# Performance work log

Measured on AMD Instinct MI355X. Metric: run time of the kernel, lower is better.

Reference implementation:

```python
import jax, jax.numpy as jnp
import numpy as np
from jax.ops import segment_sum, segment_max

N, E = 50000, 500000
F_IN, H, D1, D2, EDIM, HID = 388, 8, 64, 128, 16, 32


def gatv2(x, edge_index, edge_attr, Wl, Wr, We, att, bias, concat):
    # PyG GATv2Conv with edge_dim, add_self_loops=True, fill_value='mean', eval mode (no dropout)
    n = x.shape[0]
    h, d = att.shape
    src, dst = edge_index[0], edge_index[1]
    deg = segment_sum(jnp.ones(src.shape, x.dtype), dst, num_segments=n)
    loop_attr = segment_sum(edge_attr, dst, num_segments=n) / jnp.maximum(deg, 1.0)[:, None]
    loops = jnp.arange(n)
    src = jnp.concatenate([src, loops])
    dst = jnp.concatenate([dst, loops])
    ea = jnp.concatenate([edge_attr, loop_attr], axis=0)
    xl = (x @ Wl).reshape(n, h, d)   # source transform (lin_l)
    xr = (x @ Wr).reshape(n, h, d)   # target transform (lin_r)
    ee = (ea @ We).reshape(-1, h, d)
    m = jax.nn.leaky_relu(xl[src] + xr[dst] + ee, 0.2)   # [E+N, h, d]
    score = jnp.einsum('ehd,hd->eh', m, att)              # [E+N, h]
    smax = segment_max(score, dst, num_segments=n)        # every node has a self-loop
    alpha = jnp.exp(score - smax[dst])
    denom = segment_sum(alpha, dst, num_segments=n)
    alpha = alpha / denom[dst]
    out = segment_sum(alpha[:, :, None] * xl[src], dst, num_segments=n)  # [n, h, d]
    out = out.reshape(n, h * d) if concat else out.mean(axis=1)
    return out + bias


def setup_inputs():
    key = jax.random.key(0)
    ks = jax.random.split(key, 24)
    p = lambda k, shape: (jax.random.normal(k, shape, jnp.float32) * 0.05)
    return {
        'x': jax.random.normal(ks[0], (N, F_IN), jnp.float32),
        'edge_index': jax.random.randint(ks[1], (2, E), 0, N),
        'edge_attr': jax.random.normal(ks[2], (E, EDIM), jnp.float32),
        'Wl1': p(ks[3], (F_IN, H * D1)), 'Wr1': p(ks[4], (F_IN, H * D1)),
        'We1': p(ks[5], (EDIM, H * D1)), 'att1': p(ks[6], (H, D1)), 'b1': p(ks[7], (H * D1,)),
        'Wl2': p(ks[8], (H * D1, H * D2)), 'Wr2': p(ks[9], (H * D1, H * D2)),
        'We2': p(ks[10], (EDIM, H * D2)), 'att2': p(ks[11], (H, D2)), 'b2': p(ks[12], (D2,)),
        'W_ih': p(ks[13], (4 * HID, D2)), 'W_hh': p(ks[14], (4 * HID, HID)),
        'b_ih': p(ks[15], (4 * HID,)), 'b_hh': p(ks[16], (4 * HID,)),
        'fcW': p(ks[17], (1, HID)), 'fcb': p(ks[18], (1,)),
    }


def reference(x, edge_index, edge_attr, Wl1, Wr1, We1, att1, b1,
              Wl2, Wr2, We2, att2, b2, W_ih, W_hh, b_ih, b_hh, fcW, fcb):
    h = jnp.tanh(gatv2(x, edge_index, edge_attr, Wl1, Wr1, We1, att1, b1, True))
    h = jnp.tanh(gatv2(h, edge_index, edge_attr, Wl2, Wr2, We2, att2, b2, False))
    # single-step LSTM, h0=c0=0; W_hh @ h0 == 0 but biases remain
    gates = h @ W_ih.T + b_ih + b_hh                      # [N, 4*HID]
    i, f, g, o = jnp.split(gates, 4, axis=1)
    c = jax.nn.sigmoid(i) * jnp.tanh(g)
    hidden = jax.nn.sigmoid(o) * jnp.tanh(c)              # [N, HID]
    return hidden @ fcW.T + fcb                           # [N, 1]
```

## Files before the change

### kernel.cpp

```cpp
#include <hip/hip_runtime.h>

#define N_NODES 50000
#define N_EDGES 500000
#define F_INDIM 388
#define H_HEADS 8
#define DD1 64
#define DD2 128
#define EDIM 16
#define HIDN 32

#define M_PAD 50048
#define K1_PAD 416

typedef unsigned short u16;
typedef unsigned int u32;
typedef __attribute__((ext_vector_type(8))) short bf16x8;
typedef __attribute__((ext_vector_type(4))) float f32x4;

static __device__ __forceinline__ float bfu2f(u32 lo16) {
  union { u32 u; float f; } c;
  c.u = lo16 << 16;
  return c.f;
}
static __device__ __forceinline__ u16 f2bf(float f) {
  union { float f; u32 u; } c;
  c.f = f;
  u32 u = c.u + 0x7fffu + ((c.u >> 16) & 1u);
  return (u16)(u >> 16);
}

static __device__ __forceinline__ float waveSum(float v) {
#pragma unroll
  for (int off = 32; off > 0; off >>= 1) v += __shfl_xor(v, off, 64);
  return v;
}
static __device__ __forceinline__ void waveSum4(float& a, float& b, float& c, float& d) {
#pragma unroll
  for (int off = 32; off > 0; off >>= 1) {
    a += __shfl_xor(a, off, 64);
    b += __shfl_xor(b, off, 64);
    c += __shfl_xor(c, off, 64);
    d += __shfl_xor(d, off, 64);
  }
}

static __device__ __forceinline__ void gl_lds16(const void* g, void* l) {
  __builtin_amdgcn_global_load_lds((const __attribute__((address_space(1))) u32*)g,
                                   (__attribute__((address_space(3))) u32*)l, 16, 0, 0);
}

__global__ void k_zero(float* __restrict__ out, int n) {
  int i = blockIdx.x * blockDim.x + threadIdx.x;
  if (i < n) out[i] = 0.f;
}

__global__ void k_hist(const int* __restrict__ dst, int* __restrict__ deg) {
  int e = blockIdx.x * blockDim.x + threadIdx.x;
  if (e < N_EDGES) atomicAdd(&deg[dst[e]], 1);
}

__global__ __launch_bounds__(1024) void k_scan(const int* __restrict__ deg,
                                               int* __restrict__ row_start) {
  __shared__ int wsum[16];
  __shared__ int carry_s;
  int tid = threadIdx.x;
  int lane = tid & 63, wv = tid >> 6;
  if (tid == 0) carry_s = 0;
  __syncthreads();
  for (int base = 0; base < N_NODES; base += 1024) {
    int i = base + tid;
    int v = (i < N_NODES) ? deg[i] : 0;
    int inc = v;
#pragma unroll
    for (int off = 1; off < 64; off <<= 1) {
      int t = __shfl_up(inc, off, 64);
      if (lane >= off) inc += t;
    }
    if (lane == 63) wsum[wv] = inc;
    __syncthreads();
    if (wv == 0 && lane < 16) {
      int s = wsum[lane];
#pragma unroll
      for (int off = 1; off < 16; off <<= 1) {
        int t = __shfl_up(s, off, 64);
        if (lane >= off) s += t;
      }
      wsum[lane] = s;
    }
    __syncthreads();
    int add = (wv > 0) ? wsum[wv - 1] : 0;
    int ex = carry_s + add + inc - v;
    if (i < N_NODES) row_start[i] = ex;
    __syncthreads();
    if (tid == 0) carry_s += wsum[15];
    __syncthreads();
  }
  if (threadIdx.x == 0) row_start[N_NODES] = carry_s;
}

__global__ void k_scatter(const int* __restrict__ dst, const int* __restrict__ src,
                          const int* __restrict__ row_start, int* __restrict__ cursor,
                          int* __restrict__ eid, int* __restrict__ srcp) {
  int e = blockIdx.x * blockDim.x + threadIdx.x;
  if (e < N_EDGES) {
    int d = dst[e];
    int pos = row_start[d] + atomicAdd(&cursor[d], 1);
    eid[pos] = e;
    srcp[pos] = src[e];
  }
}

__global__ void k_cvt_x(const float* __restrict__ x, u16* __restrict__ xb) {
  long t = (long)blockIdx.x * 256 + threadIdx.x;
  if (t >= (long)M_PAD * K1_PAD) return;
  int row = (int)(t / K1_PAD);
  int col = (int)(t % K1_PAD);
  float v = (row < N_NODES && col < F_INDIM) ? x[(size_t)row * F_INDIM + col] : 0.f;
  xb[t] = f2bf(v);
}

__global__ void k_cvt_wT(const float* __restrict__ W, u16* __restrict__ WT, int K, int N, int Kp) {
  int t = blockIdx.x * 256 + threadIdx.x;
  if (t >= N * Kp) return;
  int n = t / Kp, k = t % Kp;
  WT[t] = f2bf(k < K ? W[(size_t)k * N + n] : 0.f);
}

__global__ void k_cvt(const float* __restrict__ W, u16* __restrict__ O, int n) {
  int t = blockIdx.x * 256 + threadIdx.x;
  if (t < n) O[t] = f2bf(W[t]);
}

template <bool CF32>
__global__ __launch_bounds__(256) void gemm_mfma(const u16* __restrict__ A,
                                                 const u16* __restrict__ BT,
                                                 void* __restrict__ Cv, int M, int Nd, int K,
                                                 int lda, int ldb) {
  __shared__ u16 As[128 * 32];
  __shared__ u16 Bs[128 * 32];
  int tid = threadIdx.x;
  int lane = tid & 63;
  int wv = tid >> 6;
  int m_base = blockIdx.y * 128;
  int n_base = blockIdx.x * 128;
  int wrow = (wv >> 1) * 64;
  int wcol = (wv & 1) * 64;
  f32x4 acc[4][4];
#pragma unroll
  for (int i = 0; i < 4; ++i)
#pragma unroll
    for (int j = 0; j < 4; ++j)
#pragma unroll
      for (int r = 0; r < 4; ++r) acc[i][j][r] = 0.f;

  for (int k0 = 0; k0 < K; k0 += 32) {
    __syncthreads();
#pragma unroll
    for (int it = 0; it < 2; ++it) {
      int t = it * 256 + tid;
      int row = t >> 2;
      int kc = (t & 3) * 8;
      gl_lds16(A + (size_t)(m_base + row) * lda + k0 + kc, As + (size_t)(it * 256 + wv * 64) * 8);
      gl_lds16(BT + (size_t)(n_base + row) * ldb + k0 + kc, Bs + (size_t)(it * 256 + wv * 64) * 8);
    }
    __syncthreads();
    bf16x8 af[4], bfr[4];
#pragma unroll
    for (int i = 0; i < 4; ++i) {
      int r = wrow + i * 16 + (lane & 15);
      af[i] = *(const bf16x8*)(As + r * 32 + (lane >> 4) * 8);
    }
#pragma unroll
    for (int j = 0; j < 4; ++j) {
      int r = wcol + j * 16 + (lane & 15);
      bfr[j] = *(const bf16x8*)(Bs + r * 32 + (lane >> 4) * 8);
    }
#pragma unroll
    for (int i = 0; i < 4; ++i)
#pragma unroll
      for (int j = 0; j < 4; ++j)
        acc[i][j] = __builtin_amdgcn_mfma_f32_16x16x32_bf16(af[i], bfr[j], acc[i][j], 0, 0, 0);
  }
#pragma unroll
  for (int i = 0; i < 4; ++i) {
    int grow_base = m_base + wrow + i * 16 + (lane >> 4) * 4;
#pragma unroll
    for (int j = 0; j < 4; ++j) {
      int gcol = n_base + wcol + j * 16 + (lane & 15);
#pragma unroll
      for (int r = 0; r < 4; ++r) {
        int grow = grow_base + r;
        if (grow < M) {
          float v = acc[i][j][r];
          if (CF32)
            ((float*)Cv)[(size_t)grow * Nd + gcol] = v;
          else
            ((u16*)Cv)[(size_t)grow * Nd + gcol] = f2bf(v);
        }
      }
    }
  }
}

__global__ __launch_bounds__(512) void k_gat1(
    const u16* __restrict__ xl, const u16* __restrict__ xr, const float* __restrict__ ea,
    const float* __restrict__ We, const float* __restrict__ att, const float* __restrict__ bias,
    const int* __restrict__ srcp, const int* __restrict__ eid, const int* __restrict__ row_start,
    u16* __restrict__ out) {
  const int NC = H_HEADS * DD1;
  int n = blockIdx.x;
  int tid = threadIdx.x;
  int lane = tid & 63;
  int h = tid >> 6;
  __shared__ float laP[512];
  __shared__ float la[EDIM];
  int r0 = row_start[n], r1 = row_start[n + 1];
  int deg = r1 - r0;

  {
    int k = tid & 15, i0 = tid >> 4;
    float s = 0.f;
    for (int i = i0; i < deg; i += 32) s += ea[(size_t)eid[r0 + i] * EDIM + k];
    laP[tid] = s;
  }

  int col = h * DD1 + lane;
  float Wc[EDIM];
#pragma unroll
  for (int k = 0; k < EDIM; ++k) Wc[k] = We[k * NC + col];
  float attd = att[col];
  float xrd = bfu2f(xr[(size_t)n * NC + col]);
  float xlself = bfu2f(xl[(size_t)n * NC + col]);

  auto escore = [&](int e, float xv) -> float {
    const float4* ea4 = (const float4*)(ea + (size_t)e * EDIM);
    float4 v0 = ea4[0], v1 = ea4[1], v2 = ea4[2], v3 = ea4[3];
    float eacc = v0.x * Wc[0];
    eacc = fmaf(v0.y, Wc[1], eacc);
    eacc = fmaf(v0.z, Wc[2], eacc);
    eacc = fmaf(v0.w, Wc[3], eacc);
    eacc = fmaf(v1.x, Wc[4], eacc);
    eacc = fmaf(v1.y, Wc[5], eacc);
    eacc = fmaf(v1.z, Wc[6], eacc);
    eacc = fmaf(v1.w, Wc[7], eacc);
    eacc = fmaf(v2.x, Wc[8], eacc);
    eacc = fmaf(v2.y, Wc[9], eacc);
    eacc = fmaf(v2.z, Wc[10], eacc);
    eacc = fmaf(v2.w, Wc[11], eacc);
    eacc = fmaf(v3.x, Wc[12], eacc);
    eacc = fmaf(v3.y, Wc[13], eacc);
    eacc = fmaf(v3.z, Wc[14], eacc);
    eacc = fmaf(v3.w, Wc[15], eacc);
    float zz = xv + xrd + eacc;
    float mm = zz > 0.f ? zz : 0.2f * zz;
    return mm * attd;
  };

  float acc = 0.f, denom = 0.f;
  int i = r0;
  for (; i + 4 <= r1; i += 4) {
    int e0 = eid[i], e1 = eid[i + 1], e2 = eid[i + 2], e3 = eid[i + 3];
    int s0 = srcp[i], s1 = srcp[i + 1], s2 = srcp[i + 2], s3 = srcp[i + 3];
    float x0 = bfu2f(xl[(size_t)s0 * NC + col]);
    float x1 = bfu2f(xl[(size_t)s1 * NC + col]);
    float x2 = bfu2f(xl[(size_t)s2 * NC + col]);
    float x3 = bfu2f(xl[(size_t)s3 * NC + col]);
    float p0 = escore(e0, x0);
    float p1 = escore(e1, x1);
    float p2 = escore(e2, x2);
    float p3 = escore(e3, x3);
    waveSum4(p0, p1, p2, p3);
    float w0 = __expf(p0), w1 = __expf(p1), w2 = __expf(p2), w3 = __expf(p3);
    acc = fmaf(w0, x0, acc);
    acc = fmaf(w1, x1, acc);
    acc = fmaf(w2, x2, acc);
    acc = fmaf(w3, x3, acc);
    denom += (w0 + w1) + (w2 + w3);
  }
  for (; i < r1; ++i) {
    int e = eid[i];
    int s = srcp[i];
    float xv = bfu2f(xl[(size_t)s * NC + col]);
    float p = waveSum(escore(e, xv));
    float ww = __expf(p);
    acc = fmaf(ww, xv, acc);
    denom += ww;
  }

  __syncthreads();
  if (tid < EDIM) {
    float s = 0.f;
#pragma unroll
    for (int g = 0; g < 32; ++g) s += laP[g * 16 + tid];
    la[tid] = s / (float)max(deg, 1);
  }
  __syncthreads();
  float ee = 0.f;
#pragma unroll
  for (int k = 0; k < EDIM; ++k) ee = fmaf(la[k], Wc[k], ee);
  float z = xlself + xrd + ee;
  float m = z > 0.f ? z : 0.2f * z;
  float sc = waveSum(m * attd);
  float w = __expf(sc);
  acc = fmaf(w, xlself, acc);
  denom += w;

  out[(size_t)n * NC + col] = f2bf(tanhf(acc / denom + bias[col]));
}

__global__ __launch_bounds__(512) void k_gat2(
    const u16* __restrict__ xl, const u16* __restrict__ xr, const float* __restrict__ ea,
    const float* __restrict__ We, const float* __restrict__ att, const float* __restrict__ bias,
    const int* __restrict__ srcp, const int* __restrict__ eid, const int* __restrict__ row_start,
    u16* __restrict__ out) {
  const int NC = H_HEADS * DD2;
  int n = blockIdx.x;
  int tid = threadIdx.x;
  int lane = tid & 63;
  int h = tid >> 6;
  __shared__ float laP[512];
  __shared__ float la[EDIM];
  __shared__ float hsum[H_HEADS][DD2];
  int r0 = row_start[n], r1 = row_start[n + 1];
  int deg = r1 - r0;

  {
    int k = tid & 15, i0 = tid >> 4;
    float s = 0.f;
    for (int i = i0; i < deg; i += 32) s += ea[(size_t)eid[r0 + i] * EDIM + k];
    laP[tid] = s;
  }

  int col = h * DD2 + lane * 2;
  float Wcx[EDIM], Wcy[EDIM];
#pragma unroll
  for (int k = 0; k < EDIM; ++k) {
    float2 t = *(const float2*)(We + k * NC + col);
    Wcx[k] = t.x;
    Wcy[k] = t.y;
  }
  float2 attd = *(const float2*)(att + col);
  u32 xru = *(const u32*)(xr + (size_t)n * NC + col);
  u32 xlu = *(const u32*)(xl + (size_t)n * NC + col);
  float xrdx = bfu2f(xru & 0xffff), xrdy = bfu2f(xru >> 16);
  float xlsx = bfu2f(xlu & 0xffff), xlsy = bfu2f(xlu >> 16);

  auto escore2 = [&](int e, float xvx, float xvy) -> float {
    const float4* ea4 = (const float4*)(ea + (size_t)e * EDIM);
    float4 v0 = ea4[0], v1 = ea4[1], v2 = ea4[2], v3 = ea4[3];
    float ex = v0.x * Wcx[0], ey = v0.x * Wcy[0];
    ex = fmaf(v0.y, Wcx[1], ex); ey = fmaf(v0.y, Wcy[1], ey);
    ex = fmaf(v0.z, Wcx[2], ex); ey = fmaf(v0.z, Wcy[2], ey);
    ex = fmaf(v0.w, Wcx[3], ex); ey = fmaf(v0.w, Wcy[3], ey);
    ex = fmaf(v1.x, Wcx[4], ex); ey = fmaf(v1.x, Wcy[4], ey);
    ex = fmaf(v1.y, Wcx[5], ex); ey = fmaf(v1.y, Wcy[5], ey);
    ex = fmaf(v1.z, Wcx[6], ex); ey = fmaf(v1.z, Wcy[6], ey);
    ex = fmaf(v1.w, Wcx[7], ex); ey = fmaf(v1.w, Wcy[7], ey);
    ex = fmaf(v2.x, Wcx[8], ex); ey = fmaf(v2.x, Wcy[8], ey);
    ex = fmaf(v2.y, Wcx[9], ex); ey = fmaf(v2.y, Wcy[9], ey);
    ex = fmaf(v2.z, Wcx[10], ex); ey = fmaf(v2.z, Wcy[10], ey);
    ex = fmaf(v2.w, Wcx[11], ex); ey = fmaf(v2.w, Wcy[11], ey);
    ex = fmaf(v3.x, Wcx[12], ex); ey = fmaf(v3.x, Wcy[12], ey);
    ex = fmaf(v3.y, Wcx[13], ex); ey = fmaf(v3.y, Wcy[13], ey);
    ex = fmaf(v3.z, Wcx[14], ex); ey = fmaf(v3.z, Wcy[14], ey);
    ex = fmaf(v3.w, Wcx[15], ex); ey = fmaf(v3.w, Wcy[15], ey);
    float zx = xvx + xrdx + ex, zy = xvy + xrdy + ey;
    float mx = zx > 0.f ? zx : 0.2f * zx, my = zy > 0.f ? zy : 0.2f * zy;
    return mx * attd.x + my * attd.y;
  };

  float accx = 0.f, accy = 0.f, denom = 0.f;
  int i = r0;
  for (; i + 4 <= r1; i += 4) {
    int e0 = eid[i], e1 = eid[i + 1], e2 = eid[i + 2], e3 = eid[i + 3];
    int s0 = srcp[i], s1 = srcp[i + 1], s2 = srcp[i + 2], s3 = srcp[i + 3];
    u32 u0 = *(const u32*)(xl + (size_t)s0 * NC + col);
    u32 u1 = *(const u32*)(xl + (size_t)s1 * NC + col);
    u32 u2 = *(const u32*)(xl + (size_t)s2 * NC + col);
    u32 u3 = *(const u32*)(xl + (size_t)s3 * NC + col);
    float x0x = bfu2f(u0 & 0xffff), x0y = bfu2f(u0 >> 16);
    float x1x = bfu2f(u1 & 0xffff), x1y = bfu2f(u1 >> 16);
    float x2x = bfu2f(u2 & 0xffff), x2y = bfu2f(u2 >> 16);
    float x3x = bfu2f(u3 & 0xffff), x3y = bfu2f(u3 >> 16);
    float p0 = escore2(e0, x0x, x0y);
    float p1 = escore2(e1, x1x, x1y);
    float p2 = escore2(e2, x2x, x2y);
    float p3 = escore2(e3, x3x, x3y);
    waveSum4(p0, p1, p2, p3);
    float w0 = __expf(p0), w1 = __expf(p1), w2 = __expf(p2), w3 = __expf(p3);
    accx = fmaf(w0, x0x, accx); accy = fmaf(w0, x0y, accy);
    accx = fmaf(w1, x1x, accx); accy = fmaf(w1, x1y, accy);
    accx = fmaf(w2, x2x, accx); accy = fmaf(w2, x2y, accy);
    accx = fmaf(w3, x3x, accx); accy = fmaf(w3, x3y, accy);
    denom += (w0 + w1) + (w2 + w3);
  }
  for (; i < r1; ++i) {
    int e = eid[i];
    int s = srcp[i];
    u32 u0 = *(const u32*)(xl + (size_t)s * NC + col);
    float xvx = bfu2f(u0 & 0xffff), xvy = bfu2f(u0 >> 16);
    float p = waveSum(escore2(e, xvx, xvy));
    float ww = __expf(p);
    accx = fmaf(ww, xvx, accx);
    accy = fmaf(ww, xvy, accy);
    denom += ww;
  }

  __syncthreads();
  if (tid < EDIM) {
    float s = 0.f;
#pragma unroll
    for (int g = 0; g < 32; ++g) s += laP[g * 16 + tid];
    la[tid] = s / (float)max(deg, 1);
  }
  __syncthreads();
  float eex = 0.f, eey = 0.f;
#pragma unroll
  for (int k = 0; k < EDIM; ++k) {
    eex = fmaf(la[k], Wcx[k], eex);
    eey = fmaf(la[k], Wcy[k], eey);
  }
  float zx = xlsx + xrdx + eex, zy = xlsy + xrdy + eey;
  float mx = zx > 0.f ? zx : 0.2f * zx, my = zy > 0.f ? zy : 0.2f * zy;
  float sc = waveSum(mx * attd.x + my * attd.y);
  float w = __expf(sc);
  accx = fmaf(w, xlsx, accx);
  accy = fmaf(w, xlsy, accy);
  denom += w;

  float inv = 1.f / denom;
  hsum[h][lane * 2] = accx * inv;
  hsum[h][lane * 2 + 1] = accy * inv;
  __syncthreads();
  if (tid < DD2) {
    float s = 0.f;
#pragma unroll
    for (int hh = 0; hh < H_HEADS; ++hh) s += hsum[hh][tid];
    out[(size_t)n * DD2 + tid] = f2bf(tanhf(s * 0.125f + bias[tid]));
  }
}

__global__ __launch_bounds__(128) void k_lstm(const float* __restrict__ gates,
                                              const float* __restrict__ b_ih,
                                              const float* __restrict__ b_hh,
                                              const float* __restrict__ fcW,
                                              const float* __restrict__ fcb,
                                              float* __restrict__ out) {
  int n = blockIdx.x;
  int j = threadIdx.x;
  __shared__ float gs[128];
  gs[j] = gates[(size_t)n * 128 + j] + b_ih[j] + b_hh[j];
  __syncthreads();
  if (j < 32) {
    float iv = gs[j], gv = gs[64 + j], ov = gs[96 + j];
    float c = (1.f / (1.f + __expf(-iv))) * tanhf(gv);
    float hd = (1.f / (1.f + __expf(-ov))) * tanhf(c);
    float p = hd * fcW[j];
#pragma unroll
    for (int off = 16; off > 0; off >>= 1) p += __shfl_down(p, off, 32);
    if (j == 0) out[n] = p + fcb[0];
  }
}

extern "C" void kernel_launch(void* const* d_in, const int* in_sizes, int n_in, void* d_out,
                              int out_size, void* d_ws, size_t ws_size, hipStream_t stream) {
  const float* x = (const float*)d_in[0];
  const int* ei = (const int*)d_in[1];
  const float* ea = (const float*)d_in[2];
  const float* Wl1 = (const float*)d_in[3];
  const float* Wr1 = (const float*)d_in[4];
  const float* We1 = (const float*)d_in[5];
  const float* att1 = (const float*)d_in[6];
  const float* b1 = (const float*)d_in[7];
  const float* Wl2 = (const float*)d_in[8];
  const float* Wr2 = (const float*)d_in[9];
  const float* We2 = (const float*)d_in[10];
  const float* att2 = (const float*)d_in[11];
  const float* b2 = (const float*)d_in[12];
  const float* W_ih = (const float*)d_in[13];
  const float* b_ih = (const float*)d_in[15];
  const float* b_hh = (const float*)d_in[16];
  const float* fcW = (const float*)d_in[17];
  const float* fcb = (const float*)d_in[18];
  float* out = (float*)d_out;
  const int* srcA = ei;
  const int* dstA = ei + N_EDGES;

  char* ws = (char*)d_ws;
  const size_t SZ_XL1 = (size_t)N_NODES * 512 * 2;
  const size_t SZ_P0 = (size_t)N_NODES * 1024 * 2;
  const size_t SZ_P1 = SZ_P0;
  const size_t SZ_H1 = (size_t)M_PAD * 512 * 2;
  const size_t SZ_H2 = (size_t)M_PAD * 128 * 2;
  size_t P0 = 0;
  size_t P1 = P0 + SZ_P0;
  size_t P2 = P1 + SZ_P1;
  size_t P3 = P2 + SZ_H1;
  size_t off = P3;
  auto take = [&](size_t bytes) -> char* {
    off = (off + 255) & ~(size_t)255;
    char* p = ws + off;
    off += bytes;
    return p;
  };
  u16* W1lT = (u16*)take((size_t)512 * K1_PAD * 2);
  u16* W1rT = (u16*)take((size_t)512 * K1_PAD * 2);
  u16* W2lT = (u16*)take((size_t)1024 * 512 * 2);
  u16* W2rT = (u16*)take((size_t)1024 * 512 * 2);
  u16* WihB = (u16*)take((size_t)128 * 128 * 2);
  int* deg = (int*)take((size_t)N_NODES * 4);
  int* cursor = (int*)take((size_t)N_NODES * 4);
  int* row_start = (int*)take((size_t)(N_NODES + 1) * 4);
  int* eid = (int*)take((size_t)N_EDGES * 4);
  int* srcp = (int*)take((size_t)N_EDGES * 4);

  if (off > ws_size) {
    k_zero<<<(out_size + 255) / 256, 256, 0, stream>>>(out, out_size);
    return;
  }

  u16* xl1 = (u16*)(ws + P0);
  u16* xr1 = (u16*)(ws + P0 + SZ_XL1);
  u16* xl2 = (u16*)(ws + P0);
  u16* xbf = (u16*)(ws + P1);
  u16* xr2 = (u16*)(ws + P1);
  u16* h1 = (u16*)(ws + P2);
  u16* h2 = (u16*)(ws + P2);
  float* gates = (float*)(ws + P2 + SZ_H2);

  hipMemsetAsync(deg, 0, (size_t)N_NODES * 4, stream);
  hipMemsetAsync(cursor, 0, (size_t)N_NODES * 4, stream);
  k_hist<<<(N_EDGES + 255) / 256, 256, 0, stream>>>(dstA, deg);
  k_scan<<<1, 1024, 0, stream>>>(deg, row_start);
  k_scatter<<<(N_EDGES + 255) / 256, 256, 0, stream>>>(dstA, srcA, row_start, cursor, eid, srcp);

  {
    long tot = (long)M_PAD * K1_PAD;
    k_cvt_x<<<(unsigned)((tot + 255) / 256), 256, 0, stream>>>(x, xbf);
    k_cvt_wT<<<(512 * K1_PAD + 255) / 256, 256, 0, stream>>>(Wl1, W1lT, F_INDIM, 512, K1_PAD);
    k_cvt_wT<<<(512 * K1_PAD + 255) / 256, 256, 0, stream>>>(Wr1, W1rT, F_INDIM, 512, K1_PAD);
    k_cvt_wT<<<(1024 * 512 + 255) / 256, 256, 0, stream>>>(Wl2, W2lT, 512, 1024, 512);
    k_cvt_wT<<<(1024 * 512 + 255) / 256, 256, 0, stream>>>(Wr2, W2rT, 512, 1024, 512);
    k_cvt<<<(128 * 128 + 255) / 256, 256, 0, stream>>>(W_ih, WihB, 128 * 128);
  }

  const int MB = M_PAD / 128;
  {
    dim3 g(512 / 128, MB);
    gemm_mfma<false><<<g, 256, 0, stream>>>(xbf, W1lT, xl1, N_NODES, 512, K1_PAD, K1_PAD, K1_PAD);
    gemm_mfma<false><<<g, 256, 0, stream>>>(xbf, W1rT, xr1, N_NODES, 512, K1_PAD, K1_PAD, K1_PAD);
  }
  k_gat1<<<N_NODES, 512, 0, stream>>>(xl1, xr1, ea, We1, att1, b1, srcp, eid, row_start, h1);

  {
    dim3 g(1024 / 128, MB);
    gemm_mfma<false><<<g, 256, 0, stream>>>(h1, W2lT, xl2, N_NODES, 1024, 512, 512, 512);
    gemm_mfma<false><<<g, 256, 0, stream>>>(h1, W2rT, xr2, N_NODES, 1024, 512, 512, 512);
  }
  k_gat2<<<N_NODES, 512, 0, stream>>>(xl2, xr2, ea, We2, att2, b2, srcp, eid, row_start, h2);

  {
    dim3 g(1, MB);
    gemm_mfma<true><<<g, 256, 0, stream>>>(h2, WihB, gates, N_NODES, 128, 128, 128, 128);
  }
  k_lstm<<<N_NODES, 128, 0, stream>>>(gates, b_ih, b_hh, fcW, fcb, out);
}
```

Baseline: 1.576 ms.

## Fuse lin_l/lin_r GEMMs, precompute self-loop edge means, prefetch neighbor gathers

The separate left and right projection GEMMs are merged into one GEMM over concatenated weights, writing an interleaved xl|xr buffer. The per-node mean of edge attributes for self-loops is computed once in a new kernel and shared by both GAT layers, which removes the per-block reduction and its two barriers. The GAT edge loops now use scalar (readfirstlane) edge indices, software-prefetch the next four neighbor rows, and express leaky_relu as 0.6*z+0.4*|z|. The cost is extra register pressure and a wider row stride in the gathered feature buffer.

```diff
diff --git a/kernel.cpp b/kernel.cpp
--- a/kernel.cpp
+++ b/kernel.cpp
@@ -108,6 +108,19 @@
     eid[pos] = e;
     srcp[pos] = src[e];
   }
+}
+
+__global__ __launch_bounds__(256) void k_la(const float* __restrict__ ea,
+                                            const int* __restrict__ eid,
+                                            const int* __restrict__ row_start,
+                                            float* __restrict__ la) {
+  int node = blockIdx.x * 16 + (threadIdx.x >> 4);
+  int k = threadIdx.x & 15;
+  if (node >= N_NODES) return;
+  int r0 = row_start[node], r1 = row_start[node + 1];
+  float s = 0.f;
+  for (int i = r0; i < r1; ++i) s += ea[(size_t)eid[i] * EDIM + k];
+  la[node * EDIM + k] = s / (float)max(r1 - r0, 1);
 }
 
 __global__ void k_cvt_x(const float* __restrict__ x, u16* __restrict__ xb) {
@@ -203,145 +216,136 @@
 }
 
 __global__ __launch_bounds__(512) void k_gat1(
-    const u16* __restrict__ xl, const u16* __restrict__ xr, const float* __restrict__ ea,
-    const float* __restrict__ We, const float* __restrict__ att, const float* __restrict__ bias,
-    const int* __restrict__ srcp, const int* __restrict__ eid, const int* __restrict__ row_start,
+    const u16* __restrict__ xlr, const float* __restrict__ ea, const float* __restrict__ We,
+    const float* __restrict__ att, const float* __restrict__ bias, const int* __restrict__ srcp,
+    const int* __restrict__ eid, const int* __restrict__ row_start, const float* __restrict__ la,
     u16* __restrict__ out) {
-  const int NC = H_HEADS * DD1;
+  int n = blockIdx.x;
+  int col = threadIdx.x;
+  int r0 = row_start[n], r1 = row_start[n + 1];
+  float Wc[EDIM];
+#pragma unroll
+  for (int k = 0; k < EDIM; ++k) Wc[k] = We[k * 512 + col];
+  float a = att[col];
+  float attA = 0.6f * a, attB = 0.4f * a;
+  float xrd = bfu2f(xlr[(size_t)n * 1024 + 512 + col]);
+  float xlself = bfu2f(xlr[(size_t)n * 1024 + col]);
+
+  auto escore = [&](int e, float xv) -> float {
+    const float4* ea4 = (const float4*)(ea + (size_t)e * EDIM);
+    float4 v0 = ea4[0], v1 = ea4[1], v2 = ea4[2], v3 = ea4[3];
+    float t = v0.x * Wc[0];
+    t = fmaf(v0.y, Wc[1], t);
+    t = fmaf(v0.z, Wc[2], t);
+    t = fmaf(v0.w, Wc[3], t);
+    t = fmaf(v1.x, Wc[4], t);
+    t = fmaf(v1.y, Wc[5], t);
+    t = fmaf(v1.z, Wc[6], t);
+    t = fmaf(v1.w, Wc[7], t);
+    t = fmaf(v2.x, Wc[8], t);
+    t = fmaf(v2.y, Wc[9], t);
+    t = fmaf(v2.z, Wc[10], t);
+    t = fmaf(v2.w, Wc[11], t);
+    t = fmaf(v3.x, Wc[12], t);
+    t = fmaf(v3.y, Wc[13], t);
+    t = fmaf(v3.z, Wc[14], t);
+    t = fmaf(v3.w, Wc[15], t);
+    float z = xv + xrd + t;
+    return fmaf(attA, z, attB * fabsf(z));
+  };
+
+  float acc = 0.f, denom = 0.f;
+  int iend = r0 + ((r1 - r0) & ~3);
+  int i = r0;
+  if (i < iend) {
+    int E[4], S[4];
+    float X[4];
+#pragma unroll
+    for (int r = 0; r < 4; ++r) {
+      E[r] = __builtin_amdgcn_readfirstlane(eid[i + r]);
+      S[r] = __builtin_amdgcn_readfirstlane(srcp[i + r]);
+    }
+#pragma unroll
+    for (int r = 0; r < 4; ++r) X[r] = bfu2f(xlr[(size_t)S[r] * 1024 + col]);
+    while (i < iend) {
+      int inext = i + 4;
+      int En[4], Sn[4];
+      float Xn[4];
+      bool more = inext < iend;
+      if (more) {
+#pragma unroll
+        for (int r = 0; r < 4; ++r) {
+          En[r] = __builtin_amdgcn_readfirstlane(eid[inext + r]);
+          Sn[r] = __builtin_amdgcn_readfirstlane(srcp[inext + r]);
+        }
+#pragma unroll
+        for (int r = 0; r < 4; ++r) Xn[r] = bfu2f(xlr[(size_t)Sn[r] * 1024 + col]);
+      }
+      float p0 = escore(E[0], X[0]);
+      float p1 = escore(E[1], X[1]);
+      float p2 = escore(E[2], X[2]);
+      float p3 = escore(E[3], X[3]);
+      waveSum4(p0, p1, p2, p3);
+      float w0 = __expf(p0), w1 = __expf(p1), w2 = __expf(p2), w3 = __expf(p3);
+      acc = fmaf(w0, X[0], acc);
+      acc = fmaf(w1, X[1], acc);
+      acc = fmaf(w2, X[2], acc);
+      acc = fmaf(w3, X[3], acc);
+      denom += (w0 + w1) + (w2 + w3);
+      if (more) {
+#pragma unroll
+        for (int r = 0; r < 4; ++r) {
+          E[r] = En[r];
+          S[r] = Sn[r];
+          X[r] = Xn[r];
+        }
+      }
+      i = inext;
+    }
+  }
+  for (; i < r1; ++i) {
+    int e = eid[i], s = srcp[i];
+    float xv = bfu2f(xlr[(size_t)s * 1024 + col]);
+    float p = waveSum(escore(e, xv));
+    float w = __expf(p);
+    acc = fmaf(w, xv, acc);
+    denom += w;
+  }
+  float ee = 0.f;
+#pragma unroll
+  for (int k = 0; k < EDIM; ++k) ee = fmaf(la[n * EDIM + k], Wc[k], ee);
+  float z = xlself + xrd + ee;
+  float sc = waveSum(fmaf(attA, z, attB * fabsf(z)));
+  float w = __expf(sc);
+  acc = fmaf(w, xlself, acc);
+  denom += w;
+  out[(size_t)n * 512 + col] = f2bf(tanhf(acc / denom + bias[col]));
+}
+
+__global__ __launch_bounds__(512) void k_gat2(
+    const u16* __restrict__ xlr, const float* __restrict__ ea, const float* __restrict__ We,
+    const float* __restrict__ att, const float* __restrict__ bias, const int* __restrict__ srcp,
+    const int* __restrict__ eid, const int* __restrict__ row_start, const float* __restrict__ la,
+    u16* __restrict__ out) {
   int n = blockIdx.x;
   int tid = threadIdx.x;
   int lane = tid & 63;
   int h = tid >> 6;
-  __shared__ float laP[512];
-  __shared__ float la[EDIM];
-  int r0 = row_start[n], r1 = row_start[n + 1];
-  int deg = r1 - r0;
-
-  {
-    int k = tid & 15, i0 = tid >> 4;
-    float s = 0.f;
-    for (int i = i0; i < deg; i += 32) s += ea[(size_t)eid[r0 + i] * EDIM + k];
-    laP[tid] = s;
-  }
-
-  int col = h * DD1 + lane;
-  float Wc[EDIM];
-#pragma unroll
-  for (int k = 0; k < EDIM; ++k) Wc[k] = We[k * NC + col];
-  float attd = att[col];
-  float xrd = bfu2f(xr[(size_t)n * NC + col]);
-  float xlself = bfu2f(xl[(size_t)n * NC + col]);
-
-  auto escore = [&](int e, float xv) -> float {
-    const float4* ea4 = (const float4*)(ea + (size_t)e * EDIM);
-    float4 v0 = ea4[0], v1 = ea4[1], v2 = ea4[2], v3 = ea4[3];
-    float eacc = v0.x * Wc[0];
-    eacc = fmaf(v0.y, Wc[1], eacc);
-    eacc = fmaf(v0.z, Wc[2], eacc);
-    eacc = fmaf(v0.w, Wc[3], eacc);
-    eacc = fmaf(v1.x, Wc[4], eacc);
-    eacc = fmaf(v1.y, Wc[5], eacc);
-    eacc = fmaf(v1.z, Wc[6], eacc);
-    eacc = fmaf(v1.w, Wc[7], eacc);
-    eacc = fmaf(v2.x, Wc[8], eacc);
-    eacc = fmaf(v2.y, Wc[9], eacc);
-    eacc = fmaf(v2.z, Wc[10], eacc);
-    eacc = fmaf(v2.w, Wc[11], eacc);
-    eacc = fmaf(v3.x, Wc[12], eacc);
-    eacc = fmaf(v3.y, Wc[13], eacc);
-    eacc = fmaf(v3.z, Wc[14], eacc);
-    eacc = fmaf(v3.w, Wc[15], eacc);
-    float zz = xv + xrd + eacc;
-    float mm = zz > 0.f ? zz : 0.2f * zz;
-    return mm * attd;
-  };
-
-  float acc = 0.f, denom = 0.f;
-  int i = r0;
-  for (; i + 4 <= r1; i += 4) {
-    int e0 = eid[i], e1 = eid[i + 1], e2 = eid[i + 2], e3 = eid[i + 3];
-    int s0 = srcp[i], s1 = srcp[i + 1], s2 = srcp[i + 2], s3 = srcp[i + 3];
-    float x0 = bfu2f(xl[(size_t)s0 * NC + col]);
-    float x1 = bfu2f(xl[(size_t)s1 * NC + col]);
-    float x2 = bfu2f(xl[(size_t)s2 * NC + col]);
-    float x3 = bfu2f(xl[(size_t)s3 * NC + col]);
-    float p0 = escore(e0, x0);
-    float p1 = escore(e1, x1);
-    float p2 = escore(e2, x2);
-    float p3 = escore(e3, x3);
-    waveSum4(p0, p1, p2, p3);
-    float w0 = __expf(p0), w1 = __expf(p1), w2 = __expf(p2), w3 = __expf(p3);
-    acc = fmaf(w0, x0, acc);
-    acc = fmaf(w1, x1, acc);
-    acc = fmaf(w2, x2, acc);
-    acc = fmaf(w3, x3, acc);
-    denom += (w0 + w1) + (w2 + w3);
-  }
-  for (; i < r1; ++i) {
-    int e = eid[i];
-    int s = srcp[i];
-    float xv = bfu2f(xl[(size_t)s * NC + col]);
-    float p = waveSum(escore(e, xv));
-    float ww = __expf(p);
-    acc = fmaf(ww, xv, acc);
-    denom += ww;
-  }
-
-  __syncthreads();
-  if (tid < EDIM) {
-    float s = 0.f;
-#pragma unroll
-    for (int g = 0; g < 32; ++g) s += laP[g * 16 + tid];
-    la[tid] = s / (float)max(deg, 1);
-  }
-  __syncthreads();
-  float ee = 0.f;
-#pragma unroll
-  for (int k = 0; k < EDIM; ++k) ee = fmaf(la[k], Wc[k], ee);
-  float z = xlself + xrd + ee;
-  float m = z > 0.f ? z : 0.2f * z;
-  float sc = waveSum(m * attd);
-  float w = __expf(sc);
-  acc = fmaf(w, xlself, acc);
-  denom += w;
-
-  out[(size_t)n * NC + col] = f2bf(tanhf(acc / denom + bias[col]));
-}
-
-__global__ __launch_bounds__(512) void k_gat2(
-    const u16* __restrict__ xl, const u16* __restrict__ xr, const float* __restrict__ ea,
-    const float* __restrict__ We, const float* __restrict__ att, const float* __restrict__ bias,
-    const int* __restrict__ srcp, const int* __restrict__ eid, const int* __restrict__ row_start,
-    u16* __restrict__ out) {
-  const int NC = H_HEADS * DD2;
-  int n = blockIdx.x;
-  int tid = threadIdx.x;
-  int lane = tid & 63;
-  int h = tid >> 6;
-  __shared__ float laP[512];
-  __shared__ float la[EDIM];
   __shared__ float hsum[H_HEADS][DD2];
   int r0 = row_start[n], r1 = row_start[n + 1];
-  int deg = r1 - r0;
-
-  {
-    int k = tid & 15, i0 = tid >> 4;
-    float s = 0.f;
-    for (int i = i0; i < deg; i += 32) s += ea[(size_t)eid[r0 + i] * EDIM + k];
-    laP[tid] = s;
-  }
-
   int col = h * DD2 + lane * 2;
   float Wcx[EDIM], Wcy[EDIM];
 #pragma unroll
   for (int k = 0; k < EDIM; ++k) {
-    float2 t = *(const float2*)(We + k * NC + col);
+    float2 t = *(const float2*)(We + k * 1024 + col);
     Wcx[k] = t.x;
     Wcy[k] = t.y;
   }
-  float2 attd = *(const float2*)(att + col);
-  u32 xru = *(const u32*)(xr + (size_t)n * NC + col);
-  u32 xlu = *(const u32*)(xl + (size_t)n * NC + col);
+  float2 av = *(const float2*)(att + col);
+  float attAx = 0.6f * av.x, attBx = 0.4f * av.x;
+  float attAy = 0.6f * av.y, attBy = 0.4f * av.y;
+  u32 xru = *(const u32*)(xlr + (size_t)n * 2048 + 1024 + col);
+  u32 xlu = *(const u32*)(xlr + (size_t)n * 2048 + col);
   float xrdx = bfu2f(xru & 0xffff), xrdy = bfu2f(xru >> 16);
   float xlsx = bfu2f(xlu & 0xffff), xlsy = bfu2f(xlu >> 16);
 
@@ -365,64 +369,87 @@
     ex = fmaf(v3.z, Wcx[14], ex); ey = fmaf(v3.z, Wcy[14], ey);
     ex = fmaf(v3.w, Wcx[15], ex); ey = fmaf(v3.w, Wcy[15], ey);
     float zx = xvx + xrdx + ex, zy = xvy + xrdy + ey;
-    float mx = zx > 0.f ? zx : 0.2f * zx, my = zy > 0.f ? zy : 0.2f * zy;
-    return mx * attd.x + my * attd.y;
+    float p = fmaf(attAx, zx, attBx * fabsf(zx));
+    p = fmaf(attAy, zy, p);
+    p = fmaf(attBy, fabsf(zy), p);
+    return p;
   };
 
   float accx = 0.f, accy = 0.f, denom = 0.f;
+  int iend = r0 + ((r1 - r0) & ~3);
   int i = r0;
-  for (; i + 4 <= r1; i += 4) {
-    int e0 = eid[i], e1 = eid[i + 1], e2 = eid[i + 2], e3 = eid[i + 3];
-    int s0 = srcp[i], s1 = srcp[i + 1], s2 = srcp[i + 2], s3 = srcp[i + 3];
-    u32 u0 = *(const u32*)(xl + (size_t)s0 * NC + col);
-    u32 u1 = *(const u32*)(xl + (size_t)s1 * NC + col);
-    u32 u2 = *(const u32*)(xl + (size_t)s2 * NC + col);
-    u32 u3 = *(const u32*)(xl + (size_t)s3 * NC + col);
-    float x0x = bfu2f(u0 & 0xffff), x0y = bfu2f(u0 >> 16);
-    float x1x = bfu2f(u1 & 0xffff), x1y = bfu2f(u1 >> 16);
-    float x2x = bfu2f(u2 & 0xffff), x2y = bfu2f(u2 >> 16);
-    float x3x = bfu2f(u3 & 0xffff), x3y = bfu2f(u3 >> 16);
-    float p0 = escore2(e0, x0x, x0y);
-    float p1 = escore2(e1, x1x, x1y);
-    float p2 = escore2(e2, x2x, x2y);
-    float p3 = escore2(e3, x3x, x3y);
-    waveSum4(p0, p1, p2, p3);
-    float w0 = __expf(p0), w1 = __expf(p1), w2 = __expf(p2), w3 = __expf(p3);
-    accx = fmaf(w0, x0x, accx); accy = fmaf(w0, x0y, accy);
-    accx = fmaf(w1, x1x, accx); accy = fmaf(w1, x1y, accy);
-    accx = fmaf(w2, x2x, accx); accy = fmaf(w2, x2y, accy);
-    accx = fmaf(w3, x3x, accx); accy = fmaf(w3, x3y, accy);
-    denom += (w0 + w1) + (w2 + w3);
+  if (i < iend) {
+    int E[4], S[4];
+    u32 X[4];
+#pragma unroll
+    for (int r = 0; r < 4; ++r) {
+      E[r] = __builtin_amdgcn_readfirstlane(eid[i + r]);
+      S[r] = __builtin_amdgcn_readfirstlane(srcp[i + r]);
+    }
+#pragma unroll
+    for (int r = 0; r < 4; ++r) X[r] = *(const u32*)(xlr + (size_t)S[r] * 2048 + col);
+    while (i < iend) {
+      int inext = i + 4;
+      int En[4], Sn[4];
+      u32 Xn[4];
+      bool more = inext < iend;
+      if (more) {
+#pragma unroll
+        for (int r = 0; r < 4; ++r) {
+          En[r] = __builtin_amdgcn_readfirstlane(eid[inext + r]);
+          Sn[r] = __builtin_amdgcn_readfirstlane(srcp[inext + r]);
+        }
+#pragma unroll
+        for (int r = 0; r < 4; ++r) Xn[r] = *(const u32*)(xlr + (size_t)Sn[r] * 2048 + col);
+      }
+      float x0x = bfu2f(X[0] & 0xffff), x0y = bfu2f(X[0] >> 16);
+      float x1x = bfu2f(X[1] & 0xffff), x1y = bfu2f(X[1] >> 16);
+      float x2x = bfu2f(X[2] & 0xffff), x2y = bfu2f(X[2] >> 16);
+      float x3x = bfu2f(X[3] & 0xffff), x3y = bfu2f(X[3] >> 16);
+      float p0 = escore2(E[0], x0x, x0y);
+      float p1 = escore2(E[1], x1x, x1y);
+      float p2 = escore2(E[2], x2x, x2y);
+      float p3 = escore2(E[3], x3x, x3y);
+      waveSum4(p0, p1, p2, p3);
+      float w0 = __expf(p0), w1 = __expf(p1), w2 = __expf(p2), w3 = __expf(p3);
+      accx = fmaf(w0, x0x, accx); accy = fmaf(w0, x0y, accy);
+      accx = fmaf(w1, x1x, accx); accy = fmaf(w1, x1y, accy);
+      accx = fmaf(w2, x2x, accx); accy = fmaf(w2, x2y, accy);
+      accx = fmaf(w3, x3x, accx); accy = fmaf(w3, x3y, accy);
+      denom += (w0 + w1) + (w2 + w3);
+      if (more) {
+#pragma unroll
+        for (int r = 0; r < 4; ++r) {
+          E[r] = En[r];
+          S[r] = Sn[r];
+          X[r] = Xn[r];
+        }
+      }
+      i = inext;
+    }
   }
   for (; i < r1; ++i) {
-    int e = eid[i];
-    int s = srcp[i];
-    u32 u0 = *(const u32*)(xl + (size_t)s * NC + col);
+    int e = eid[i], s = srcp[i];
+    u32 u0 = *(const u32*)(xlr + (size_t)s * 2048 + col);
     float xvx = bfu2f(u0 & 0xffff), xvy = bfu2f(u0 >> 16);
     float p = waveSum(escore2(e, xvx, xvy));
-    float ww = __expf(p);
-    accx = fmaf(ww, xvx, accx);
-    accy = fmaf(ww, xvy, accy);
-    denom += ww;
-  }
-
-  __syncthreads();
-  if (tid < EDIM) {
-    float s = 0.f;
-#pragma unroll
-    for (int g = 0; g < 32; ++g) s += laP[g * 16 + tid];
-    la[tid] = s / (float)max(deg, 1);
-  }
-  __syncthreads();
+    float w = __expf(p);
+    accx = fmaf(w, xvx, accx);
+    accy = fmaf(w, xvy, accy);
+    denom += w;
+  }
   float eex = 0.f, eey = 0.f;
 #pragma unroll
   for (int k = 0; k < EDIM; ++k) {
-    eex = fmaf(la[k], Wcx[k], eex);
-    eey = fmaf(la[k], Wcy[k], eey);
+    float lv = la[n * EDIM + k];
+    eex = fmaf(lv, Wcx[k], eex);
+    eey = fmaf(lv, Wcy[k], eey);
   }
   float zx = xlsx + xrdx + eex, zy = xlsy + xrdy + eey;
-  float mx = zx > 0.f ? zx : 0.2f * zx, my = zy > 0.f ? zy : 0.2f * zy;
-  float sc = waveSum(mx * attd.x + my * attd.y);
+  float ps = fmaf(attAx, zx, attBx * fabsf(zx));
+  ps = fmaf(attAy, zy, ps);
+  ps = fmaf(attBy, fabsf(zy), ps);
+  float sc = waveSum(ps);
   float w = __expf(sc);
   accx = fmaf(w, xlsx, accx);
   accy = fmaf(w, xlsy, accy);
@@ -487,81 +514,66 @@
   const int* dstA = ei + N_EDGES;
 
   char* ws = (char*)d_ws;
-  const size_t SZ_XL1 = (size_t)N_NODES * 512 * 2;
-  const size_t SZ_P0 = (size_t)N_NODES * 1024 * 2;
-  const size_t SZ_P1 = SZ_P0;
-  const size_t SZ_H1 = (size_t)M_PAD * 512 * 2;
-  const size_t SZ_H2 = (size_t)M_PAD * 128 * 2;
-  size_t P0 = 0;
-  size_t P1 = P0 + SZ_P0;
-  size_t P2 = P1 + SZ_P1;
-  size_t P3 = P2 + SZ_H1;
-  size_t off = P3;
+  const size_t OFF_XBF = (size_t)N_NODES * 1024 * 2;
+  const size_t OFF_H1 = (size_t)N_NODES * 2048 * 2;
+  const size_t OFF_GATES = OFF_H1 + (size_t)M_PAD * 128 * 2;
+  size_t off = OFF_H1 + (size_t)M_PAD * 512 * 2;
   auto take = [&](size_t bytes) -> char* {
     off = (off + 255) & ~(size_t)255;
     char* p = ws + off;
     off += bytes;
     return p;
   };
-  u16* W1lT = (u16*)take((size_t)512 * K1_PAD * 2);
-  u16* W1rT = (u16*)take((size_t)512 * K1_PAD * 2);
-  u16* W2lT = (u16*)take((size_t)1024 * 512 * 2);
-  u16* W2rT = (u16*)take((size_t)1024 * 512 * 2);
+  u16* W1T = (u16*)take((size_t)1024 * K1_PAD * 2);
+  u16* W2T = (u16*)take((size_t)2048 * 512 * 2);
   u16* WihB = (u16*)take((size_t)128 * 128 * 2);
   int* deg = (int*)take((size_t)N_NODES * 4);
   int* cursor = (int*)take((size_t)N_NODES * 4);
   int* row_start = (int*)take((size_t)(N_NODES + 1) * 4);
   int* eid = (int*)take((size_t)N_EDGES * 4);
   int* srcp = (int*)take((size_t)N_EDGES * 4);
+  float* la = (float*)take((size_t)N_NODES * EDIM * 4);
 
   if (off > ws_size) {
     k_zero<<<(out_size + 255) / 256, 256, 0, stream>>>(out, out_size);
     return;
   }
 
-  u16* xl1 = (u16*)(ws + P0);
-  u16* xr1 = (u16*)(ws + P0 + SZ_XL1);
-  u16* xl2 = (u16*)(ws + P0);
-  u16* xbf = (u16*)(ws + P1);
-  u16* xr2 = (u16*)(ws + P1);
-  u16* h1 = (u16*)(ws + P2);
-  u16* h2 = (u16*)(ws + P2);
-  float* gates = (float*)(ws + P2 + SZ_H2);
+  u16* xlr1 = (u16*)ws;
+  u16* xbf = (u16*)(ws + OFF_XBF);
+  u16* xlr2 = (u16*)ws;
+  u16* h1 = (u16*)(ws + OFF_H1);
+  u16* h2 = (u16*)(ws + OFF_H1);
+  float* gates = (float*)(ws + OFF_GATES);
 
   hipMemsetAsync(deg, 0, (size_t)N_NODES * 4, stream);
   hipMemsetAsync(cursor, 0, (size_t)N_NODES * 4, stream);
   k_hist<<<(N_EDGES + 255) / 256, 256, 0, stream>>>(dstA, deg);
   k_scan<<<1, 1024, 0, stream>>>(deg, row_start);
   k_scatter<<<(N_EDGES + 255) / 256, 256, 0, stream>>>(dstA, srcA, row_start, cursor, eid, srcp);
+  k_la<<<(N_NODES + 15) / 16, 256, 0, stream>>>(ea, eid, row_start, la);
 
   {
     long tot = (long)M_PAD * K1_PAD;
     k_cvt_x<<<(unsigned)((tot + 255) / 256), 256, 0, stream>>>(x, xbf);
-    k_cvt_wT<<<(512 * K1_PAD + 255) / 256, 256, 0, stream>>>(Wl1, W1lT, F_INDIM, 512, K1_PAD);
-    k_cvt_wT<<<(512 * K1_PAD + 255) / 256, 256, 0, stream>>>(Wr1, W1rT, F_INDIM, 512, K1_PAD);
-    k_cvt_wT<<<(1024 * 512 + 255) / 256, 256, 0, stream>>>(Wl2, W2lT, 512, 1024, 512);
-    k_cvt_wT<<<(1024 * 512 + 255) / 256, 256, 0, stream>>>(Wr2, W2rT, 512, 1024, 512);
+    k_cvt_wT<<<(512 * K1_PAD + 255) / 256, 256, 0, stream>>>(Wl1, W1T, F_INDIM, 512, K1_PAD);
+    k_cvt_wT<<<(512 * K1_PAD + 255) / 256, 256, 0, stream>>>(Wr1, W1T + (size_t)512 * K1_PAD,
+                                                             F_INDIM, 512, K1_PAD);
+    k_cvt_wT<<<(1024 * 512 + 255) / 256, 256, 0, stream>>>(Wl2, W2T, 512, 1024, 512);
+    k_cvt_wT<<<(1024 * 512 + 255) / 256, 256, 0, stream>>>(Wr2, W2T + (size_t)1024 * 512, 512,
+                                                           1024, 512);
     k_cvt<<<(128 * 128 + 255) / 256, 256, 0, stream>>>(W_ih, WihB, 128 * 128);
   }
 
   const int MB = M_PAD / 128;
-  {
-    dim3 g(512 / 128, MB);
-    gemm_mfma<false><<<g, 256, 0, stream>>>(xbf, W1lT, xl1, N_NODES, 512, K1_PAD, K1_PAD, K1_PAD);
-    gemm_mfma<false><<<g, 256, 0, stream>>>(xbf, W1rT, xr1, N_NODES, 512, K1_PAD, K1_PAD, K1_PAD);
-  }
-  k_gat1<<<N_NODES, 512, 0, stream>>>(xl1, xr1, ea, We1, att1, b1, srcp, eid, row_start, h1);
-
-  {
-    dim3 g(1024 / 128, MB);
-    gemm_mfma<false><<<g, 256, 0, stream>>>(h1, W2lT, xl2, N_NODES, 1024, 512, 512, 512);
-    gemm_mfma<false><<<g, 256, 0, stream>>>(h1, W2rT, xr2, N_NODES, 1024, 512, 512, 512);
-  }
-  k_gat2<<<N_NODES, 512, 0, stream>>>(xl2, xr2, ea, We2, att2, b2, srcp, eid, row_start, h2);
-
-  {
-    dim3 g(1, MB);
-    gemm_mfma<true><<<g, 256, 0, stream>>>(h2, WihB, gates, N_NODES, 128, 128, 128, 128);
-  }
+  gemm_mfma<false><<<dim3(1024 / 128, MB), 256, 0, stream>>>(xbf, W1T, xlr1, N_NODES, 1024,
+                                                             K1_PAD, K1_PAD, K1_PAD);
+  k_gat1<<<N_NODES, 512, 0, stream>>>(xlr1, ea, We1, att1, b1, srcp, eid, row_start, la, h1);
+
+  gemm_mfma<false><<<dim3(2048 / 128, MB), 256, 0, stream>>>(h1, W2T, xlr2, N_NODES, 2048, 512,
+                                                             512, 512);
+  k_gat2<<<N_NODES, 512, 0, stream>>>(xlr2, ea, We2, att2, b2, srcp, eid, row_start, la, h2);
+
+  gemm_mfma<true><<<dim3(1, MB), 256, 0, stream>>>(h2, WihB, gates, N_NODES, 128, 128, 128, 128);
   k_lstm<<<N_NODES, 128, 0, stream>>>(gates, b_ih, b_hh, fcW, fcb, out);
 }
```

Result: slower. 1.683 ms (+6.8%).
